# Kernel optimization log

Hardware: AMD Instinct MI355X
Metric: run time of the kernel (lower is better)

## Reference

```python
import jax, jax.numpy as jnp
import numpy as np

D_STATE = 8
D_CONV = 4
DT_RANK = 8
THRESHOLD = 0.5
KPOOL = 3
PAD = (KPOOL - 1) // 2
EPS = 1e-5


def _rmsnorm(x, w):
    return x * jax.lax.rsqrt(jnp.mean(x * x, axis=-1, keepdims=True) + EPS) * w


def _dw_causal_conv(x, w, b):
    # x: (L, T, C), w: (C, 1, K) depthwise causal conv along T
    xt = jnp.transpose(x, (0, 2, 1))  # (L, C, T)
    y = jax.lax.conv_general_dilated(
        xt, w, window_strides=(1,), padding=[(D_CONV - 1, 0)],
        dimension_numbers=('NCH', 'OIH', 'NCH'), feature_group_count=xt.shape[1])
    return jnp.transpose(y, (0, 2, 1)) + b


def _selective_scan(x, delta, A, B, Cm, D):
    # x, delta: (L,T,d); A: (d,n); B, Cm: (L,T,n); D: (d,)
    dA = jnp.exp(delta[..., None] * A)                        # (L,T,d,n)
    dBx = (delta * x)[..., None] * B[:, :, None, :]           # (L,T,d,n)
    def combine(a, b):
        a1, b1 = a
        a2, b2 = b
        return (a2 * a1, a2 * b1 + b2)
    _, h = jax.lax.associative_scan(combine, (dA, dBx), axis=1)
    y = jnp.einsum('ltdn,ltn->ltd', h, Cm)
    return y + x * D


def _mamba_block(x, in_proj, conv_w, conv_b, x_proj_w, dt_proj_w, dt_proj_b,
                 A_log_f, A_log_b, D_f, D_b, out_proj_w, rms_w):
    # single-depth bidirectional (bimamba-v2 style) block, expand=1, residual + RMSNorm
    res = x
    xn = _rmsnorm(x, rms_w)
    xz = xn @ in_proj                       # (L,T,2C)
    xi, z = jnp.split(xz, 2, axis=-1)
    xi = jax.nn.silu(_dw_causal_conv(xi, conv_w, conv_b))
    dbl = xi @ x_proj_w                     # (L,T,dt_rank+2*d_state)
    dt = dbl[..., :DT_RANK]
    Bm = dbl[..., DT_RANK:DT_RANK + D_STATE]
    Cm = dbl[..., DT_RANK + D_STATE:]
    delta = jax.nn.softplus(dt @ dt_proj_w + dt_proj_b)
    A_f = -jnp.exp(A_log_f)
    A_b = -jnp.exp(A_log_b)
    flip = lambda a: a[:, ::-1]
    y_f = _selective_scan(xi, delta, A_f, Bm, Cm, D_f)
    y_b = flip(_selective_scan(flip(xi), flip(delta), A_b, flip(Bm), flip(Cm), D_b))
    y = 0.5 * (y_f + y_b) * jax.nn.silu(z)  # if_devide_out -> average two directions
    return res + y @ out_proj_w


def reference(feats, in_proj, conv_w, conv_b, x_proj_w, dt_proj_w, dt_proj_b,
              A_log_f, A_log_b, D_f, D_b, out_proj_w, rms_w, mlp_w, mlp_b,
              record_len):
    N, C, H, W = feats.shape
    T = H * W
    rec = np.asarray(record_len)  # static ragged group sizes
    ends = np.cumsum(rec)
    starts = ends - rec
    masks = []
    for s0, L in zip(starts.tolist(), rec.tolist()):
        g = feats[s0:s0 + L]                       # (L,C,H,W)
        if L > 1:
            x = g.reshape(L, C, T).transpose(0, 2, 1)  # l c h w -> l (h w) c
            feat = _mamba_block(x, in_proj, conv_w, conv_b, x_proj_w, dt_proj_w,
                                dt_proj_b, A_log_f, A_log_b, D_f, D_b,
                                out_proj_w, rms_w)
            score = jax.nn.sigmoid(feat @ mlp_w + mlp_b)   # (L,T,1)
            ego = jnp.ones((1, T, 1), feats.dtype)
            bs = jnp.concatenate([ego, score[1:]], axis=0)
        else:
            bs = jnp.ones((1, T, 1), feats.dtype)
        bs = bs.transpose(0, 2, 1).reshape(L, 1, H, W)     # l (h w) c -> l c h w
        masks.append(jnp.where(bs > THRESHOLD, 1.0, 0.0).astype(feats.dtype))
    mask = jnp.concatenate(masks, axis=0)                  # (N,1,H,W)
    pooled = jax.lax.reduce_window(
        mask, -jnp.inf, jax.lax.max,
        window_dimensions=(1, 1, KPOOL, KPOOL), window_strides=(1, 1, 1, 1),
        padding=[(0, 0), (0, 0), (PAD, PAD), (PAD, PAD)])
    return pooled


def setup_inputs():
    key = jax.random.key(0)
    ks = jax.random.split(key, 8)
    C, H, W = 128, 96, 96
    record_len = np.array([2, 3, 1, 2, 4], dtype=np.int64)
    N = int(record_len.sum())
    s = 0.05
    A_log = jnp.log(jnp.broadcast_to(
        jnp.arange(1, D_STATE + 1, dtype=jnp.float32), (C, D_STATE)))
    return {
        'feats': jax.random.normal(ks[0], (N, C, H, W), jnp.float32),
        'in_proj': jax.random.normal(ks[1], (C, 2 * C), jnp.float32) * s,
        'conv_w': jax.random.normal(ks[2], (C, 1, D_CONV), jnp.float32) * s,
        'conv_b': jnp.zeros((C,), jnp.float32),
        'x_proj_w': jax.random.normal(ks[3], (C, DT_RANK + 2 * D_STATE), jnp.float32) * s,
        'dt_proj_w': jax.random.normal(ks[4], (DT_RANK, C), jnp.float32) * s,
        'dt_proj_b': jnp.full((C,), 0.1, jnp.float32),
        'A_log_f': A_log,
        'A_log_b': A_log,
        'D_f': jnp.ones((C,), jnp.float32),
        'D_b': jnp.ones((C,), jnp.float32),
        'out_proj_w': jax.random.normal(ks[5], (C, C), jnp.float32) * s,
        'rms_w': jnp.ones((C,), jnp.float32),
        'mlp_w': jax.random.normal(ks[6], (C, 1), jnp.float32) * s,
        'mlp_b': jnp.zeros((1,), jnp.float32),
        'record_len': jnp.asarray(record_len),
    }
```

## Files before the change

### kernel.cpp

```cpp
#include <hip/hip_runtime.h>
#include <cstdint>
#include <cstddef>

#define C_CH 128
#define T_TOK 9216
#define H_IMG 96
#define W_IMG 96
#define NSTATE 8

#define CHUNK 64
#define RHALO 32

__device__ __forceinline__ float siluf_dev(float x) {
  return x / (1.0f + expf(-x));
}

__global__ __launch_bounds__(128) void k0_setup(
    const int* __restrict__ rec, int n_groups, int N,
    const float* __restrict__ out_proj_w, const float* __restrict__ mlp_w,
    float* __restrict__ vvec, int* __restrict__ slot)
{
  const int tid = threadIdx.x;
  if (tid == 0) {
    int f = 0, sl = 0;
    for (int g = 0; g < n_groups; ++g) {
      const int L = rec[g];
      slot[f] = -1;
      for (int i = 1; i < L; ++i) slot[f + i] = sl++;
      f += L;
    }
  }
  if (tid < C_CH) {
    float acc = 0.0f;
    for (int j = 0; j < C_CH; ++j) acc += out_proj_w[tid * C_CH + j] * mlp_w[j];
    vvec[tid] = acc;
  }
}

__global__ __launch_bounds__(256) void k1_gemm(
    const float* __restrict__ feats, const float* __restrict__ in_proj,
    const float* __restrict__ rms_w, const float* __restrict__ mlp_w,
    const float* __restrict__ mlp_b, const float* __restrict__ vvec,
    const int* __restrict__ slot,
    float* __restrict__ xipre, float* __restrict__ wbuf,
    float* __restrict__ logit)
{
  __shared__ float Asm[C_CH * 64];
  __shared__ float Bsm[C_CH * 64];
  __shared__ float redA[256], redB[256], irS[64];
  const int f = blockIdx.y;
  const int s = slot[f];
  if (s < 0) return;
  const int m0 = blockIdx.x * 64;
  const int tid = threadIdx.x;

  {
    const int c0 = tid >> 4;
    const int tq = (tid & 15) * 4;
    const float* src = feats + (size_t)f * C_CH * T_TOK + m0 + tq;
    #pragma unroll
    for (int i = 0; i < 8; ++i) {
      const int c = c0 + i * 16;
      const float4 x4 = *(const float4*)(src + (size_t)c * T_TOK);
      *(float4*)&Asm[c * 64 + tq] = x4;
    }
  }
  __syncthreads();
  {
    const int t = tid & 63;
    const int q = tid >> 6;
    float ssum = 0.0f, rm = 0.0f;
    for (int cc = q * 32; cc < q * 32 + 32; ++cc) {
      const float val = Asm[cc * 64 + t];
      ssum += val * val;
      rm += val * mlp_w[cc];
    }
    redA[tid] = ssum; redB[tid] = rm;
  }
  __syncthreads();
  if (tid < 64) {
    const int t = tid;
    const float ssum = redA[t] + redA[t + 64] + redA[t + 128] + redA[t + 192];
    const float rm   = redB[t] + redB[t + 64] + redB[t + 128] + redB[t + 192];
    const float ir = 1.0f / sqrtf(ssum * (1.0f / C_CH) + 1e-5f);
    logit[(size_t)s * T_TOK + m0 + t] = rm + mlp_b[0];
    irS[t] = ir;
  }
  __syncthreads();
  {
    const int t = tid & 63;
    const int q = tid >> 6;
    const float ir = irS[t];
    for (int cc = q * 32; cc < q * 32 + 32; ++cc) Asm[cc * 64 + t] *= ir;
  }

  const int ti = tid >> 4;
  const int tc = tid & 15;
  for (int chunk = 0; chunk < 4; ++chunk) {
    const int n0 = chunk * 64;
    __syncthreads();
    #pragma unroll
    for (int i = 0; i < 8; ++i) {
      const int idx = tid + 256 * i;
      const int k = idx >> 4;
      const int q = (idx & 15) * 4;
      float4 b4 = *(const float4*)(in_proj + (size_t)k * 256 + n0 + q);
      const float rw = rms_w[k];
      b4.x *= rw; b4.y *= rw; b4.z *= rw; b4.w *= rw;
      *(float4*)&Bsm[k * 64 + q] = b4;
    }
    __syncthreads();
    float acc[4][4];
    #pragma unroll
    for (int i = 0; i < 4; ++i)
      #pragma unroll
      for (int j = 0; j < 4; ++j) acc[i][j] = 0.0f;
    #pragma unroll 8
    for (int k = 0; k < C_CH; ++k) {
      const float4 a4 = *(const float4*)&Asm[k * 64 + ti * 4];
      const float4 b4 = *(const float4*)&Bsm[k * 64 + tc * 4];
      acc[0][0] += a4.x * b4.x; acc[0][1] += a4.x * b4.y; acc[0][2] += a4.x * b4.z; acc[0][3] += a4.x * b4.w;
      acc[1][0] += a4.y * b4.x; acc[1][1] += a4.y * b4.y; acc[1][2] += a4.y * b4.z; acc[1][3] += a4.y * b4.w;
      acc[2][0] += a4.z * b4.x; acc[2][1] += a4.z * b4.y; acc[2][2] += a4.z * b4.z; acc[2][3] += a4.z * b4.w;
      acc[3][0] += a4.w * b4.x; acc[3][1] += a4.w * b4.y; acc[3][2] += a4.w * b4.z; acc[3][3] += a4.w * b4.w;
    }
    if (chunk < 2) {
      const int cb = n0 + tc * 4;
      #pragma unroll
      for (int i = 0; i < 4; ++i) {
        const int t = m0 + ti * 4 + i;
        float4 o; o.x = acc[i][0]; o.y = acc[i][1]; o.z = acc[i][2]; o.w = acc[i][3];
        *(float4*)&xipre[((size_t)s * T_TOK + t) * C_CH + cb] = o;
      }
    } else {
      const int zc = (chunk - 2) * 64 + tc * 4;
      const float4 v4 = *(const float4*)&vvec[zc];
      #pragma unroll
      for (int i = 0; i < 4; ++i) {
        const int t = m0 + ti * 4 + i;
        float4 o;
        o.x = 0.5f * siluf_dev(acc[i][0]) * v4.x;
        o.y = 0.5f * siluf_dev(acc[i][1]) * v4.y;
        o.z = 0.5f * siluf_dev(acc[i][2]) * v4.z;
        o.w = 0.5f * siluf_dev(acc[i][3]) * v4.w;
        *(float4*)&wbuf[((size_t)s * T_TOK + t) * C_CH + zc] = o;
      }
    }
  }
}

__global__ __launch_bounds__(256, 3) void k3_fused(
    const float* __restrict__ xipre, const float* __restrict__ wbuf,
    const float* __restrict__ conv_w, const float* __restrict__ conv_b,
    const float* __restrict__ x_proj_w,
    const float* __restrict__ dt_proj_w, const float* __restrict__ dt_proj_b,
    const float* __restrict__ A_log_f, const float* __restrict__ A_log_b,
    const float* __restrict__ D_f, const float* __restrict__ D_b,
    const int* __restrict__ slot, float* __restrict__ logit)
{
  __shared__ float xibuf[64 * 129];
  __shared__ float dbl[128 * 24];
  const int f = blockIdx.y;
  const int s = slot[f];
  if (s < 0) return;
  const int c0 = blockIdx.x * CHUNK;
  const int r0 = c0 - RHALO;
  const int tid = threadIdx.x;
  const int c = tid & 127;
  const int half = tid >> 7;
  const size_t rowbase = (size_t)s * T_TOK;
  const float4 cw = *(const float4*)(conv_w + c * 4);
  const float cb = conv_b[c];

  auto ldx = [&](int t) -> float {
    return (t >= 0 && t < T_TOK) ? xipre[(rowbase + t) * C_CH + c] : 0.0f;
  };

  const int q6 = __builtin_amdgcn_readfirstlane(tid >> 6) * 6;
  const int tok = tid & 63;
  for (int pass = 0; pass < 2; ++pass) {
    __syncthreads();
    {
      const int prow0 = pass * 64 + half * 32;
      float xm1 = ldx(r0 + prow0 - 1);
      float xm2 = ldx(r0 + prow0 - 2);
      float xm3 = ldx(r0 + prow0 - 3);
      for (int i = 0; i < 32; ++i) {
        const float cur = ldx(r0 + prow0 + i);
        const float sum = cw.x * xm3 + cw.y * xm2 + cw.z * xm1 + cw.w * cur + cb;
        xibuf[(half * 32 + i) * 129 + c] = sum / (1.0f + __expf(-sum));
        xm3 = xm2; xm2 = xm1; xm1 = cur;
      }
    }
    __syncthreads();
    {
      float acc[6] = {0, 0, 0, 0, 0, 0};
      for (int cc = 0; cc < C_CH; ++cc) {
        const float xv = xibuf[tok * 129 + cc];
        #pragma unroll
        for (int jj = 0; jj < 6; ++jj)
          acc[jj] += xv * x_proj_w[cc * 24 + q6 + jj];
      }
      #pragma unroll
      for (int jj = 0; jj < 6; ++jj)
        dbl[(pass * 64 + tok) * 24 + q6 + jj] = acc[jj];
    }
  }
  __syncthreads();

  float dw[8], Ac[8];
  const float* Alog = half ? A_log_b : A_log_f;
  #pragma unroll
  for (int r = 0; r < 8; ++r) dw[r] = dt_proj_w[r * C_CH + c];
  #pragma unroll
  for (int n = 0; n < NSTATE; ++n) Ac[n] = -expf(Alog[c * NSTATE + n]);
  const float bias = dt_proj_b[c];
  const float Dd = half ? D_b[c] : D_f[c];
  float h[8] = {0, 0, 0, 0, 0, 0, 0, 0};

  if (half == 0) {
    const int tb = (r0 < 0) ? 0 : r0;
    const int steps = c0 + CHUNK - tb;
    const int outg0 = (c0 - tb) >> 3;
    const int ng = steps >> 3;
    float xm1 = ldx(tb - 1), xm2 = ldx(tb - 2), xm3 = ldx(tb - 3);
    for (int g = 0; g < ng; ++g) {
      const int t0 = tb + g * 8;
      const bool out = (g >= outg0);
      float pg[8], wg[8];
      #pragma unroll
      for (int j = 0; j < 8; ++j) {
        const size_t gi = (rowbase + t0 + j) * C_CH + c;
        pg[j] = xipre[gi];
        wg[j] = out ? wbuf[gi] : 0.0f;
      }
      #pragma unroll
      for (int j = 0; j < 8; ++j) {
        const int t = t0 + j;
        const int p = t - r0;
        const float cur = pg[j];
        const float sum = cw.x * xm3 + cw.y * xm2 + cw.z * xm1 + cw.w * cur + cb;
        const float xiv = sum / (1.0f + __expf(-sum));
        xm3 = xm2; xm2 = xm1; xm1 = cur;
        const float4 d0 = *(const float4*)&dbl[p * 24];
        const float4 d1 = *(const float4*)&dbl[p * 24 + 4];
        float pre = bias;
        pre += d0.x * dw[0] + d0.y * dw[1] + d0.z * dw[2] + d0.w * dw[3];
        pre += d1.x * dw[4] + d1.y * dw[5] + d1.z * dw[6] + d1.w * dw[7];
        const float dlt = fmaxf(pre, 0.0f) + __logf(1.0f + __expf(-fabsf(pre)));
        const float u = dlt * xiv;
        const float4 b0 = *(const float4*)&dbl[p * 24 + 8];
        const float4 b1 = *(const float4*)&dbl[p * 24 + 12];
        h[0] = __expf(dlt * Ac[0]) * h[0] + u * b0.x;
        h[1] = __expf(dlt * Ac[1]) * h[1] + u * b0.y;
        h[2] = __expf(dlt * Ac[2]) * h[2] + u * b0.z;
        h[3] = __expf(dlt * Ac[3]) * h[3] + u * b0.w;
        h[4] = __expf(dlt * Ac[4]) * h[4] + u * b1.x;
        h[5] = __expf(dlt * Ac[5]) * h[5] + u * b1.y;
        h[6] = __expf(dlt * Ac[6]) * h[6] + u * b1.z;
        h[7] = __expf(dlt * Ac[7]) * h[7] + u * b1.w;
        if (out) {
          const float4 cc0 = *(const float4*)&dbl[p * 24 + 16];
          const float4 cc1 = *(const float4*)&dbl[p * 24 + 20];
          float y = xiv * Dd;
          y += h[0] * cc0.x + h[1] * cc0.y + h[2] * cc0.z + h[3] * cc0.w;
          y += h[4] * cc1.x + h[5] * cc1.y + h[6] * cc1.z + h[7] * cc1.w;
          float contrib = y * wg[j];
          contrib += __shfl_xor(contrib, 1);
          contrib += __shfl_xor(contrib, 2);
          contrib += __shfl_xor(contrib, 4);
          contrib += __shfl_xor(contrib, 8);
          contrib += __shfl_xor(contrib, 16);
          contrib += __shfl_xor(contrib, 32);
          if ((tid & 63) == 0) atomicAdd(&logit[rowbase + t], contrib);
        }
      }
    }
  } else {
    const int te2e = r0 + 128;
    const int te2 = (te2e > T_TOK) ? T_TOK : te2e;
    const int steps = te2 - c0;
    const int outg0 = (te2 - (c0 + CHUNK)) >> 3;
    const int ng = steps >> 3;
    float w0 = ldx(te2 - 1), w1 = ldx(te2 - 2), w2 = ldx(te2 - 3), w3 = ldx(te2 - 4);
    for (int g = 0; g < ng; ++g) {
      const int t0 = te2 - 1 - g * 8;
      const bool out = (g >= outg0);
      float nv[8], wg[8];
      #pragma unroll
      for (int j = 0; j < 8; ++j) {
        nv[j] = ldx(t0 - 4 - j);
        wg[j] = out ? wbuf[(rowbase + t0 - j) * C_CH + c] : 0.0f;
      }
      #pragma unroll
      for (int j = 0; j < 8; ++j) {
        const int t = t0 - j;
        const int p = t - r0;
        const float sum = cw.x * w3 + cw.y * w2 + cw.z * w1 + cw.w * w0 + cb;
        const float xiv = sum / (1.0f + __expf(-sum));
        w0 = w1; w1 = w2; w2 = w3; w3 = nv[j];
        const float4 d0 = *(const float4*)&dbl[p * 24];
        const float4 d1 = *(const float4*)&dbl[p * 24 + 4];
        float pre = bias;
        pre += d0.x * dw[0] + d0.y * dw[1] + d0.z * dw[2] + d0.w * dw[3];
        pre += d1.x * dw[4] + d1.y * dw[5] + d1.z * dw[6] + d1.w * dw[7];
        const float dlt = fmaxf(pre, 0.0f) + __logf(1.0f + __expf(-fabsf(pre)));
        const float u = dlt * xiv;
        const float4 b0 = *(const float4*)&dbl[p * 24 + 8];
        const float4 b1 = *(const float4*)&dbl[p * 24 + 12];
        h[0] = __expf(dlt * Ac[0]) * h[0] + u * b0.x;
        h[1] = __expf(dlt * Ac[1]) * h[1] + u * b0.y;
        h[2] = __expf(dlt * Ac[2]) * h[2] + u * b0.z;
        h[3] = __expf(dlt * Ac[3]) * h[3] + u * b0.w;
        h[4] = __expf(dlt * Ac[4]) * h[4] + u * b1.x;
        h[5] = __expf(dlt * Ac[5]) * h[5] + u * b1.y;
        h[6] = __expf(dlt * Ac[6]) * h[6] + u * b1.z;
        h[7] = __expf(dlt * Ac[7]) * h[7] + u * b1.w;
        if (out) {
          const float4 cc0 = *(const float4*)&dbl[p * 24 + 16];
          const float4 cc1 = *(const float4*)&dbl[p * 24 + 20];
          float y = xiv * Dd;
          y += h[0] * cc0.x + h[1] * cc0.y + h[2] * cc0.z + h[3] * cc0.w;
          y += h[4] * cc1.x + h[5] * cc1.y + h[6] * cc1.z + h[7] * cc1.w;
          float contrib = y * wg[j];
          contrib += __shfl_xor(contrib, 1);
          contrib += __shfl_xor(contrib, 2);
          contrib += __shfl_xor(contrib, 4);
          contrib += __shfl_xor(contrib, 8);
          contrib += __shfl_xor(contrib, 16);
          contrib += __shfl_xor(contrib, 32);
          if ((tid & 63) == 0) atomicAdd(&logit[rowbase + t], contrib);
        }
      }
    }
  }
}

__global__ __launch_bounds__(128) void k4_pool(
    const float* __restrict__ logit, const int* __restrict__ slot,
    float* __restrict__ out)
{
  const int w = threadIdx.x;
  if (w >= W_IMG) return;
  const int hh = blockIdx.x;
  const int f = blockIdx.y;
  const int s = slot[f];
  float m = 0.0f;
  if (s < 0) {
    m = 1.0f;
  } else {
    for (int dh = -1; dh <= 1; ++dh) {
      const int h2 = hh + dh;
      if (h2 < 0 || h2 >= H_IMG) continue;
      for (int dw = -1; dw <= 1; ++dw) {
        const int w2 = w + dw;
        if (w2 < 0 || w2 >= W_IMG) continue;
        if (logit[(size_t)s * T_TOK + h2 * W_IMG + w2] > 0.0f) m = 1.0f;
      }
    }
  }
  out[(size_t)f * T_TOK + hh * W_IMG + w] = m;
}

extern "C" void kernel_launch(void* const* d_in, const int* in_sizes, int n_in,
                              void* d_out, int out_size, void* d_ws, size_t ws_size,
                              hipStream_t stream) {
  const float* feats      = (const float*)d_in[0];
  const float* in_proj    = (const float*)d_in[1];
  const float* conv_w     = (const float*)d_in[2];
  const float* conv_b     = (const float*)d_in[3];
  const float* x_proj_w   = (const float*)d_in[4];
  const float* dt_proj_w  = (const float*)d_in[5];
  const float* dt_proj_b  = (const float*)d_in[6];
  const float* A_log_f    = (const float*)d_in[7];
  const float* A_log_b    = (const float*)d_in[8];
  const float* D_f        = (const float*)d_in[9];
  const float* D_b        = (const float*)d_in[10];
  const float* out_proj_w = (const float*)d_in[11];
  const float* rms_w      = (const float*)d_in[12];
  const float* mlp_w      = (const float*)d_in[13];
  const float* mlp_b      = (const float*)d_in[14];
  const int*   rec        = (const int*)d_in[15];

  const int N = in_sizes[0] / (C_CH * T_TOK);
  const int n_groups = in_sizes[15];
  int S = N - n_groups;
  if (S < 1) S = 1;

  char* p = (char*)d_ws;
  float* vvec  = (float*)p; p += 1024;
  int*   slot  = (int*)p;   p += ((N * 4 + 255) / 256) * 256;
  float* logit = (float*)p; p += (size_t)S * T_TOK * 4;
  float* xipre = (float*)p; p += (size_t)S * T_TOK * C_CH * 4;
  float* wA    = (float*)p; p += (size_t)S * T_TOK * C_CH * 4;
  (void)ws_size; (void)n_in; (void)out_size;

  k0_setup<<<1, 128, 0, stream>>>(rec, n_groups, N, out_proj_w, mlp_w, vvec, slot);
  k1_gemm<<<dim3(T_TOK / 64, N), 256, 0, stream>>>(
      feats, in_proj, rms_w, mlp_w, mlp_b, vvec, slot, xipre, wA, logit);
  k3_fused<<<dim3(T_TOK / CHUNK, N), 256, 0, stream>>>(
      xipre, wA, conv_w, conv_b, x_proj_w, dt_proj_w, dt_proj_b,
      A_log_f, A_log_b, D_f, D_b, slot, logit);
  k4_pool<<<dim3(H_IMG, N), 128, 0, stream>>>(logit, slot, (float*)d_out);
}
```

Baseline: 367.6 us.

## Retile input GEMM, precompute scaled weights, shrink scan smem, reuse exp powers

The input-projection GEMM now uses 128x128 output tiles with K-slicing and an 8x8 register tile per thread. It splits the x and z halves across a grid dimension and applies the RMS scaling in the epilogue instead of rescaling the A tile in shared memory. The rms_w-scaled in_proj is precomputed once in the setup kernel. The fused scan kernel halves its xibuf shared buffer to raise occupancy, at the cost of four convolution passes with half the threads idle in the x_proj step. When A rows form the sequence n*A0, detected at runtime by a ballot, one exp plus repeated multiplies replace eight exps; this exploits the test's A_log initialisation and risks some rounding drift.

```diff
diff --git a/kernel.cpp b/kernel.cpp
--- a/kernel.cpp
+++ b/kernel.cpp
@@ -11,14 +11,19 @@
 #define CHUNK 64
 #define RHALO 32
 
+#define MT 128
+#define NT 128
+#define KS 32
+
 __device__ __forceinline__ float siluf_dev(float x) {
   return x / (1.0f + expf(-x));
 }
 
-__global__ __launch_bounds__(128) void k0_setup(
+__global__ __launch_bounds__(256) void k0_setup(
     const int* __restrict__ rec, int n_groups, int N,
     const float* __restrict__ out_proj_w, const float* __restrict__ mlp_w,
-    float* __restrict__ vvec, int* __restrict__ slot)
+    const float* __restrict__ in_proj, const float* __restrict__ rms_w,
+    float* __restrict__ vvec, int* __restrict__ slot, float* __restrict__ Bf)
 {
   const int tid = threadIdx.x;
   if (tid == 0) {
@@ -35,121 +40,125 @@
     for (int j = 0; j < C_CH; ++j) acc += out_proj_w[tid * C_CH + j] * mlp_w[j];
     vvec[tid] = acc;
   }
-}
-
-__global__ __launch_bounds__(256) void k1_gemm(
-    const float* __restrict__ feats, const float* __restrict__ in_proj,
-    const float* __restrict__ rms_w, const float* __restrict__ mlp_w,
-    const float* __restrict__ mlp_b, const float* __restrict__ vvec,
-    const int* __restrict__ slot,
+  for (int idx = tid; idx < C_CH * 256; idx += 256) {
+    const int k = idx >> 8;
+    Bf[idx] = in_proj[idx] * rms_w[k];
+  }
+}
+
+__global__ __launch_bounds__(256, 4) void k1_gemm(
+    const float* __restrict__ feats, const float* __restrict__ Bf,
+    const float* __restrict__ mlp_w, const float* __restrict__ mlp_b,
+    const float* __restrict__ vvec, const int* __restrict__ slot,
     float* __restrict__ xipre, float* __restrict__ wbuf,
     float* __restrict__ logit)
 {
-  __shared__ float Asm[C_CH * 64];
-  __shared__ float Bsm[C_CH * 64];
-  __shared__ float redA[256], redB[256], irS[64];
-  const int f = blockIdx.y;
+  __shared__ float Asm[KS * MT];
+  __shared__ float Bsm[KS * NT];
+  __shared__ float redS[256], redR[256], irS[MT];
+  const int f = blockIdx.z;
   const int s = slot[f];
   if (s < 0) return;
-  const int m0 = blockIdx.x * 64;
+  const int m0 = blockIdx.x * MT;
+  const int nch = blockIdx.y;
+  const int j0 = nch * NT;
   const int tid = threadIdx.x;
-
-  {
-    const int c0 = tid >> 4;
-    const int tq = (tid & 15) * 4;
-    const float* src = feats + (size_t)f * C_CH * T_TOK + m0 + tq;
+  const int tm = tid & 15;
+  const int tn = tid >> 4;
+  const size_t fbase = (size_t)f * C_CH * T_TOK;
+  const size_t rowbase = (size_t)s * T_TOK;
+
+  float acc[8][8];
+  #pragma unroll
+  for (int i = 0; i < 8; ++i)
+    #pragma unroll
+    for (int j = 0; j < 8; ++j) acc[i][j] = 0.0f;
+  float ssum = 0.0f, rmsum = 0.0f;
+  const int tokA = tid & 127;
+  const int khalf = tid >> 7;
+
+  for (int ks = 0; ks < 4; ++ks) {
+    const int k0 = ks * KS;
+    __syncthreads();
+    #pragma unroll
+    for (int i = 0; i < 4; ++i) {
+      const int idx = tid + 256 * i;
+      const int r = idx >> 5;
+      const int q = (idx & 31) * 4;
+      *(float4*)&Asm[r * MT + q] =
+          *(const float4*)&feats[fbase + (size_t)(k0 + r) * T_TOK + m0 + q];
+      *(float4*)&Bsm[r * NT + q] =
+          *(const float4*)&Bf[(k0 + r) * 256 + j0 + q];
+    }
+    __syncthreads();
+    #pragma unroll
+    for (int kk = 0; kk < 16; ++kk) {
+      const int k = khalf * 16 + kk;
+      const float v = Asm[k * MT + tokA];
+      ssum = fmaf(v, v, ssum);
+      rmsum = fmaf(v, mlp_w[k0 + k], rmsum);
+    }
+    #pragma unroll 8
+    for (int k = 0; k < KS; ++k) {
+      const float4 a0 = *(const float4*)&Asm[k * MT + tm * 8];
+      const float4 a1 = *(const float4*)&Asm[k * MT + tm * 8 + 4];
+      const float4 b0 = *(const float4*)&Bsm[k * NT + tn * 8];
+      const float4 b1 = *(const float4*)&Bsm[k * NT + tn * 8 + 4];
+      const float ar[8] = {a0.x, a0.y, a0.z, a0.w, a1.x, a1.y, a1.z, a1.w};
+      const float br[8] = {b0.x, b0.y, b0.z, b0.w, b1.x, b1.y, b1.z, b1.w};
+      #pragma unroll
+      for (int i = 0; i < 8; ++i)
+        #pragma unroll
+        for (int j = 0; j < 8; ++j)
+          acc[i][j] = fmaf(ar[i], br[j], acc[i][j]);
+    }
+  }
+  redS[tid] = ssum; redR[tid] = rmsum;
+  __syncthreads();
+  if (tid < 128) {
+    const float ss = redS[tid] + redS[tid + 128];
+    irS[tid] = 1.0f / sqrtf(ss * (1.0f / C_CH) + 1e-5f);
+    if (nch == 0)
+      logit[rowbase + m0 + tid] = redR[tid] + redR[tid + 128] + mlp_b[0];
+  }
+  __syncthreads();
+
+  if (nch == 0) {
     #pragma unroll
     for (int i = 0; i < 8; ++i) {
-      const int c = c0 + i * 16;
-      const float4 x4 = *(const float4*)(src + (size_t)c * T_TOK);
-      *(float4*)&Asm[c * 64 + tq] = x4;
-    }
-  }
-  __syncthreads();
-  {
-    const int t = tid & 63;
-    const int q = tid >> 6;
-    float ssum = 0.0f, rm = 0.0f;
-    for (int cc = q * 32; cc < q * 32 + 32; ++cc) {
-      const float val = Asm[cc * 64 + t];
-      ssum += val * val;
-      rm += val * mlp_w[cc];
-    }
-    redA[tid] = ssum; redB[tid] = rm;
-  }
-  __syncthreads();
-  if (tid < 64) {
-    const int t = tid;
-    const float ssum = redA[t] + redA[t + 64] + redA[t + 128] + redA[t + 192];
-    const float rm   = redB[t] + redB[t + 64] + redB[t + 128] + redB[t + 192];
-    const float ir = 1.0f / sqrtf(ssum * (1.0f / C_CH) + 1e-5f);
-    logit[(size_t)s * T_TOK + m0 + t] = rm + mlp_b[0];
-    irS[t] = ir;
-  }
-  __syncthreads();
-  {
-    const int t = tid & 63;
-    const int q = tid >> 6;
-    const float ir = irS[t];
-    for (int cc = q * 32; cc < q * 32 + 32; ++cc) Asm[cc * 64 + t] *= ir;
-  }
-
-  const int ti = tid >> 4;
-  const int tc = tid & 15;
-  for (int chunk = 0; chunk < 4; ++chunk) {
-    const int n0 = chunk * 64;
-    __syncthreads();
+      const int t = m0 + tm * 8 + i;
+      const float irv = irS[tm * 8 + i];
+      float4 o0, o1;
+      o0.x = acc[i][0] * irv; o0.y = acc[i][1] * irv;
+      o0.z = acc[i][2] * irv; o0.w = acc[i][3] * irv;
+      o1.x = acc[i][4] * irv; o1.y = acc[i][5] * irv;
+      o1.z = acc[i][6] * irv; o1.w = acc[i][7] * irv;
+      float* dst = &xipre[(rowbase + t) * C_CH + tn * 8];
+      *(float4*)dst = o0;
+      *(float4*)(dst + 4) = o1;
+    }
+  } else {
+    const float4 v0 = *(const float4*)&vvec[tn * 8];
+    const float4 v1 = *(const float4*)&vvec[tn * 8 + 4];
+    const float vr[8] = {v0.x, v0.y, v0.z, v0.w, v1.x, v1.y, v1.z, v1.w};
     #pragma unroll
     for (int i = 0; i < 8; ++i) {
-      const int idx = tid + 256 * i;
-      const int k = idx >> 4;
-      const int q = (idx & 15) * 4;
-      float4 b4 = *(const float4*)(in_proj + (size_t)k * 256 + n0 + q);
-      const float rw = rms_w[k];
-      b4.x *= rw; b4.y *= rw; b4.z *= rw; b4.w *= rw;
-      *(float4*)&Bsm[k * 64 + q] = b4;
-    }
-    __syncthreads();
-    float acc[4][4];
-    #pragma unroll
-    for (int i = 0; i < 4; ++i)
-      #pragma unroll
-      for (int j = 0; j < 4; ++j) acc[i][j] = 0.0f;
-    #pragma unroll 8
-    for (int k = 0; k < C_CH; ++k) {
-      const float4 a4 = *(const float4*)&Asm[k * 64 + ti * 4];
-      const float4 b4 = *(const float4*)&Bsm[k * 64 + tc * 4];
-      acc[0][0] += a4.x * b4.x; acc[0][1] += a4.x * b4.y; acc[0][2] += a4.x * b4.z; acc[0][3] += a4.x * b4.w;
-      acc[1][0] += a4.y * b4.x; acc[1][1] += a4.y * b4.y; acc[1][2] += a4.y * b4.z; acc[1][3] += a4.y * b4.w;
-      acc[2][0] += a4.z * b4.x; acc[2][1] += a4.z * b4.y; acc[2][2] += a4.z * b4.z; acc[2][3] += a4.z * b4.w;
-      acc[3][0] += a4.w * b4.x; acc[3][1] += a4.w * b4.y; acc[3][2] += a4.w * b4.z; acc[3][3] += a4.w * b4.w;
-    }
-    if (chunk < 2) {
-      const int cb = n0 + tc * 4;
-      #pragma unroll
-      for (int i = 0; i < 4; ++i) {
-        const int t = m0 + ti * 4 + i;
-        float4 o; o.x = acc[i][0]; o.y = acc[i][1]; o.z = acc[i][2]; o.w = acc[i][3];
-        *(float4*)&xipre[((size_t)s * T_TOK + t) * C_CH + cb] = o;
-      }
-    } else {
-      const int zc = (chunk - 2) * 64 + tc * 4;
-      const float4 v4 = *(const float4*)&vvec[zc];
-      #pragma unroll
-      for (int i = 0; i < 4; ++i) {
-        const int t = m0 + ti * 4 + i;
-        float4 o;
-        o.x = 0.5f * siluf_dev(acc[i][0]) * v4.x;
-        o.y = 0.5f * siluf_dev(acc[i][1]) * v4.y;
-        o.z = 0.5f * siluf_dev(acc[i][2]) * v4.z;
-        o.w = 0.5f * siluf_dev(acc[i][3]) * v4.w;
-        *(float4*)&wbuf[((size_t)s * T_TOK + t) * C_CH + zc] = o;
-      }
-    }
-  }
-}
-
-__global__ __launch_bounds__(256, 3) void k3_fused(
+      const int t = m0 + tm * 8 + i;
+      const float irv = irS[tm * 8 + i];
+      float o[8];
+      #pragma unroll
+      for (int j = 0; j < 8; ++j) {
+        const float z = acc[i][j] * irv;
+        o[j] = 0.5f * (z / (1.0f + __expf(-z))) * vr[j];
+      }
+      float* dst = &wbuf[(rowbase + t) * C_CH + tn * 8];
+      *(float4*)dst = *(float4*)&o[0];
+      *(float4*)(dst + 4) = *(float4*)&o[4];
+    }
+  }
+}
+
+__global__ __launch_bounds__(256, 5) void k3_fused(
     const float* __restrict__ xipre, const float* __restrict__ wbuf,
     const float* __restrict__ conv_w, const float* __restrict__ conv_b,
     const float* __restrict__ x_proj_w,
@@ -158,7 +167,7 @@
     const float* __restrict__ D_f, const float* __restrict__ D_b,
     const int* __restrict__ slot, float* __restrict__ logit)
 {
-  __shared__ float xibuf[64 * 129];
+  __shared__ float xibuf[32 * 129];
   __shared__ float dbl[128 * 24];
   const int f = blockIdx.y;
   const int s = slot[f];
@@ -178,22 +187,22 @@
 
   const int q6 = __builtin_amdgcn_readfirstlane(tid >> 6) * 6;
   const int tok = tid & 63;
-  for (int pass = 0; pass < 2; ++pass) {
+  for (int pass = 0; pass < 4; ++pass) {
     __syncthreads();
     {
-      const int prow0 = pass * 64 + half * 32;
-      float xm1 = ldx(r0 + prow0 - 1);
-      float xm2 = ldx(r0 + prow0 - 2);
-      float xm3 = ldx(r0 + prow0 - 3);
-      for (int i = 0; i < 32; ++i) {
-        const float cur = ldx(r0 + prow0 + i);
+      const int pr0 = pass * 32 + half * 16;
+      float xm1 = ldx(r0 + pr0 - 1);
+      float xm2 = ldx(r0 + pr0 - 2);
+      float xm3 = ldx(r0 + pr0 - 3);
+      for (int i = 0; i < 16; ++i) {
+        const float cur = ldx(r0 + pr0 + i);
         const float sum = cw.x * xm3 + cw.y * xm2 + cw.z * xm1 + cw.w * cur + cb;
-        xibuf[(half * 32 + i) * 129 + c] = sum / (1.0f + __expf(-sum));
+        xibuf[(half * 16 + i) * 129 + c] = sum / (1.0f + __expf(-sum));
         xm3 = xm2; xm2 = xm1; xm1 = cur;
       }
     }
     __syncthreads();
-    {
+    if (tok < 32) {
       float acc[6] = {0, 0, 0, 0, 0, 0};
       for (int cc = 0; cc < C_CH; ++cc) {
         const float xv = xibuf[tok * 129 + cc];
@@ -203,7 +212,7 @@
       }
       #pragma unroll
       for (int jj = 0; jj < 6; ++jj)
-        dbl[(pass * 64 + tok) * 24 + q6 + jj] = acc[jj];
+        dbl[(pass * 32 + tok) * 24 + q6 + jj] = acc[jj];
     }
   }
   __syncthreads();
@@ -214,6 +223,11 @@
   for (int r = 0; r < 8; ++r) dw[r] = dt_proj_w[r * C_CH + c];
   #pragma unroll
   for (int n = 0; n < NSTATE; ++n) Ac[n] = -expf(Alog[c * NSTATE + n]);
+  bool fa = true;
+  #pragma unroll
+  for (int n = 0; n < NSTATE; ++n)
+    fa = fa && (fabsf(Ac[n] - (n + 1) * Ac[0]) < 1e-5f * (n + 1));
+  const bool fast = (__ballot(fa) == 0xFFFFFFFFFFFFFFFFull);
   const float bias = dt_proj_b[c];
   const float Dd = half ? D_b[c] : D_f[c];
   float h[8] = {0, 0, 0, 0, 0, 0, 0, 0};
@@ -249,16 +263,21 @@
         pre += d1.x * dw[4] + d1.y * dw[5] + d1.z * dw[6] + d1.w * dw[7];
         const float dlt = fmaxf(pre, 0.0f) + __logf(1.0f + __expf(-fabsf(pre)));
         const float u = dlt * xiv;
+        float e[8];
+        if (fast) {
+          const float r1 = __expf(dlt * Ac[0]);
+          e[0] = r1; e[1] = r1 * r1; e[2] = e[1] * r1; e[3] = e[2] * r1;
+          e[4] = e[3] * r1; e[5] = e[4] * r1; e[6] = e[5] * r1; e[7] = e[6] * r1;
+        } else {
+          #pragma unroll
+          for (int n = 0; n < 8; ++n) e[n] = __expf(dlt * Ac[n]);
+        }
         const float4 b0 = *(const float4*)&dbl[p * 24 + 8];
         const float4 b1 = *(const float4*)&dbl[p * 24 + 12];
-        h[0] = __expf(dlt * Ac[0]) * h[0] + u * b0.x;
-        h[1] = __expf(dlt * Ac[1]) * h[1] + u * b0.y;
-        h[2] = __expf(dlt * Ac[2]) * h[2] + u * b0.z;
-        h[3] = __expf(dlt * Ac[3]) * h[3] + u * b0.w;
-        h[4] = __expf(dlt * Ac[4]) * h[4] + u * b1.x;
-        h[5] = __expf(dlt * Ac[5]) * h[5] + u * b1.y;
-        h[6] = __expf(dlt * Ac[6]) * h[6] + u * b1.z;
-        h[7] = __expf(dlt * Ac[7]) * h[7] + u * b1.w;
+        h[0] = e[0] * h[0] + u * b0.x; h[1] = e[1] * h[1] + u * b0.y;
+        h[2] = e[2] * h[2] + u * b0.z; h[3] = e[3] * h[3] + u * b0.w;
+        h[4] = e[4] * h[4] + u * b1.x; h[5] = e[5] * h[5] + u * b1.y;
+        h[6] = e[6] * h[6] + u * b1.z; h[7] = e[7] * h[7] + u * b1.w;
         if (out) {
           const float4 cc0 = *(const float4*)&dbl[p * 24 + 16];
           const float4 cc1 = *(const float4*)&dbl[p * 24 + 20];
@@ -306,16 +325,21 @@
         pre += d1.x * dw[4] + d1.y * dw[5] + d1.z * dw[6] + d1.w * dw[7];
         const float dlt = fmaxf(pre, 0.0f) + __logf(1.0f + __expf(-fabsf(pre)));
         const float u = dlt * xiv;
+        float e[8];
+        if (fast) {
+          const float r1 = __expf(dlt * Ac[0]);
+          e[0] = r1; e[1] = r1 * r1; e[2] = e[1] * r1; e[3] = e[2] * r1;
+          e[4] = e[3] * r1; e[5] = e[4] * r1; e[6] = e[5] * r1; e[7] = e[6] * r1;
+        } else {
+          #pragma unroll
+          for (int n = 0; n < 8; ++n) e[n] = __expf(dlt * Ac[n]);
+        }
         const float4 b0 = *(const float4*)&dbl[p * 24 + 8];
         const float4 b1 = *(const float4*)&dbl[p * 24 + 12];
-        h[0] = __expf(dlt * Ac[0]) * h[0] + u * b0.x;
-        h[1] = __expf(dlt * Ac[1]) * h[1] + u * b0.y;
-        h[2] = __expf(dlt * Ac[2]) * h[2] + u * b0.z;
-        h[3] = __expf(dlt * Ac[3]) * h[3] + u * b0.w;
-        h[4] = __expf(dlt * Ac[4]) * h[4] + u * b1.x;
-        h[5] = __expf(dlt * Ac[5]) * h[5] + u * b1.y;
-        h[6] = __expf(dlt * Ac[6]) * h[6] + u * b1.z;
-        h[7] = __expf(dlt * Ac[7]) * h[7] + u * b1.w;
+        h[0] = e[0] * h[0] + u * b0.x; h[1] = e[1] * h[1] + u * b0.y;
+        h[2] = e[2] * h[2] + u * b0.z; h[3] = e[3] * h[3] + u * b0.w;
+        h[4] = e[4] * h[4] + u * b1.x; h[5] = e[5] * h[5] + u * b1.y;
+        h[6] = e[6] * h[6] + u * b1.z; h[7] = e[7] * h[7] + u * b1.w;
         if (out) {
           const float4 cc0 = *(const float4*)&dbl[p * 24 + 16];
           const float4 cc1 = *(const float4*)&dbl[p * 24 + 20];
@@ -390,14 +414,16 @@
   char* p = (char*)d_ws;
   float* vvec  = (float*)p; p += 1024;
   int*   slot  = (int*)p;   p += ((N * 4 + 255) / 256) * 256;
+  float* Bf    = (float*)p; p += C_CH * 256 * 4;
   float* logit = (float*)p; p += (size_t)S * T_TOK * 4;
   float* xipre = (float*)p; p += (size_t)S * T_TOK * C_CH * 4;
   float* wA    = (float*)p; p += (size_t)S * T_TOK * C_CH * 4;
   (void)ws_size; (void)n_in; (void)out_size;
 
-  k0_setup<<<1, 128, 0, stream>>>(rec, n_groups, N, out_proj_w, mlp_w, vvec, slot);
-  k1_gemm<<<dim3(T_TOK / 64, N), 256, 0, stream>>>(
-      feats, in_proj, rms_w, mlp_w, mlp_b, vvec, slot, xipre, wA, logit);
+  k0_setup<<<1, 256, 0, stream>>>(rec, n_groups, N, out_proj_w, mlp_w,
+                                  in_proj, rms_w, vvec, slot, Bf);
+  k1_gemm<<<dim3(T_TOK / MT, 2, N), 256, 0, stream>>>(
+      feats, Bf, mlp_w, mlp_b, vvec, slot, xipre, wA, logit);
   k3_fused<<<dim3(T_TOK / CHUNK, N), 256, 0, stream>>>(
       xipre, wA, conv_w, conv_b, x_proj_w, dt_proj_w, dt_proj_b,
       A_log_f, A_log_b, D_f, D_b, slot, logit);
```

After: 372.1 us. About the same (+1.2%).
